# Performance work log

Hardware: AMD Instinct MI355X
Metric: run time of the kernel (lower is better)

The kernel has to match this reference:

```python
import jax, jax.numpy as jnp
import numpy as np

N = 16384      # nodes
E = 524288     # edges (avg degree 32)
F_IN, H1, H2 = 256, 64, 32


def _spmm(edge_src, edge_dst, edge_weight, h):
    """Sparse A @ h with A given as COO edge list: out[i] = sum_{e: src==i} w_e * h[dst_e]."""
    msg = h[edge_dst] * edge_weight[:, None]          # [E, d] gather + scale
    return jax.ops.segment_sum(msg, edge_src, num_segments=N)


def setup_inputs() -> dict:
    key = jax.random.key(0)
    ks = jax.random.split(key, 9)
    x = jax.random.normal(ks[0], (N, F_IN), dtype=jnp.float32)
    edge_src = jax.random.randint(ks[1], (E,), 0, N, dtype=jnp.int32)
    edge_dst = jax.random.randint(ks[2], (E,), 0, N, dtype=jnp.int32)
    edge_weight = jax.random.uniform(ks[3], (E,), dtype=jnp.float32)
    # Xavier-uniform GCN weights
    def xavier(k, shape):
        lim = np.sqrt(6.0 / (shape[0] + shape[1])).astype(np.float32)
        return jax.random.uniform(k, shape, jnp.float32, -lim, lim)
    W1 = xavier(ks[4], (F_IN, H1))
    W2 = xavier(ks[5], (H1, H2))
    W3 = xavier(ks[6], (H1, H2))
    R = jax.random.normal(ks[7], (H2,), dtype=jnp.float32)           # DEDICOM diagonal
    M = jnp.diag(jax.random.normal(ks[8], (H2,), dtype=jnp.float32))  # initialized as diag(randn)
    return dict(x=x, edge_weight=edge_weight, W1=W1, W2=W2, W3=W3, R=R, M=M,
                edge_src=edge_src, edge_dst=edge_dst)


def reference(x, edge_weight, W1, W2, W3, R, M, edge_src, edge_dst):
    # GCN propagation A @ (X @ W); stored activations are never applied in the
    # original ConvGraph.forward, so none are applied here. Eval mode: no
    # dropout, reparameterize returns z_mean.
    h = _spmm(edge_src, edge_dst, edge_weight, x @ W1)        # [N, H1]
    z_mean = _spmm(edge_src, edge_dst, edge_weight, h @ W2)   # [N, H2]
    z_log_std = _spmm(edge_src, edge_dst, edge_weight, h @ W3)
    z = z_mean
    # DEDICOM decoder (act = identity): zt = z @ diag(R) @ M @ diag(R); out = zt @ zt.T
    zt = ((z * R[None, :]) @ M) * R[None, :]                  # diag matmuls -> elementwise scales
    adj_pred = zt @ zt.T                                      # [N, N]
    return adj_pred, z_mean, z_log_std
```

## Files before the change

kernel.cpp:

```cpp
#include <hip/hip_runtime.h>
#include <hip/hip_bf16.h>

#define NN 16384
#define NE 524288
#define FIN 256
#define HH1 64
#define HH2 32

typedef __attribute__((ext_vector_type(8))) short bf16x8;
typedef __attribute__((ext_vector_type(4))) float f32x4;

__global__ __launch_bounds__(256) void zero_ints(int* __restrict__ p, int n) {
  int i = blockIdx.x * 256 + threadIdx.x;
  if (i < n) p[i] = 0;
}

__global__ __launch_bounds__(256) void gemm_xw1(const float* __restrict__ x,
                                                const float* __restrict__ W1,
                                                float* __restrict__ H0) {
  __shared__ float xs[64][65];
  __shared__ float ws[64][65];
  const int t = threadIdx.x;
  const int row0 = blockIdx.x * 64;
  const int tr = t >> 4, tc = t & 15;
  float acc[4][4] = {};
  for (int kc = 0; kc < FIN; kc += 64) {
#pragma unroll
    for (int i = 0; i < 4; ++i) {
      int slot = t + i * 256;
      int r = slot >> 4, c4 = (slot & 15) * 4;
      float4 v = *reinterpret_cast<const float4*>(&x[(size_t)(row0 + r) * FIN + kc + c4]);
      xs[r][c4 + 0] = v.x; xs[r][c4 + 1] = v.y; xs[r][c4 + 2] = v.z; xs[r][c4 + 3] = v.w;
      float4 wv = *reinterpret_cast<const float4*>(&W1[(size_t)(kc + r) * HH1 + c4]);
      ws[r][c4 + 0] = wv.x; ws[r][c4 + 1] = wv.y; ws[r][c4 + 2] = wv.z; ws[r][c4 + 3] = wv.w;
    }
    __syncthreads();
#pragma unroll
    for (int k = 0; k < 64; ++k) {
      float a[4], b[4];
#pragma unroll
      for (int i = 0; i < 4; ++i) a[i] = xs[tr * 4 + i][k];
#pragma unroll
      for (int j = 0; j < 4; ++j) b[j] = ws[k][tc * 4 + j];
#pragma unroll
      for (int i = 0; i < 4; ++i)
#pragma unroll
        for (int j = 0; j < 4; ++j) acc[i][j] += a[i] * b[j];
    }
    __syncthreads();
  }
#pragma unroll
  for (int i = 0; i < 4; ++i) {
    float4 o; o.x = acc[i][0]; o.y = acc[i][1]; o.z = acc[i][2]; o.w = acc[i][3];
    *reinterpret_cast<float4*>(&H0[(size_t)(row0 + tr * 4 + i) * HH1 + tc * 4]) = o;
  }
}

__global__ __launch_bounds__(256) void hist_src(const int* __restrict__ src,
                                                int* __restrict__ cnt) {
  int e = blockIdx.x * 256 + threadIdx.x;
  if (e < NE) atomicAdd(&cnt[src[e]], 1);
}

__global__ __launch_bounds__(256) void scan_offsets(const int* __restrict__ cnt,
                                                    int* __restrict__ off,
                                                    int* __restrict__ cur) {
  __shared__ int sums[256];
  const int t = threadIdx.x;
  const int base = t * 64;
  int s = 0;
  for (int i = 0; i < 64; ++i) s += cnt[base + i];
  sums[t] = s;
  __syncthreads();
  if (t == 0) {
    int run = 0;
    for (int i = 0; i < 256; ++i) { int v = sums[i]; sums[i] = run; run += v; }
  }
  __syncthreads();
  int run = sums[t];
  for (int i = 0; i < 64; ++i) {
    off[base + i] = run;
    cur[base + i] = run;
    run += cnt[base + i];
  }
  if (t == 255) off[NN] = run;
}

__global__ __launch_bounds__(256) void scatter_edges(const int* __restrict__ src,
                                                     const int* __restrict__ dst,
                                                     const float* __restrict__ w,
                                                     int* __restrict__ cur,
                                                     int* __restrict__ sdst,
                                                     float* __restrict__ sw) {
  int e = blockIdx.x * 256 + threadIdx.x;
  if (e < NE) {
    int s = src[e];
    int p = atomicAdd(&cur[s], 1);
    sdst[p] = dst[e];
    sw[p] = w[e];
  }
}

__global__ __launch_bounds__(256) void spmm64(const int* __restrict__ off,
                                              const int* __restrict__ sdst,
                                              const float* __restrict__ sw,
                                              const float* __restrict__ Hin,
                                              float* __restrict__ Hout) {
  const int node = blockIdx.x * 4 + (threadIdx.x >> 6);
  const int lane = threadIdx.x & 63;
  const int beg = off[node], end = off[node + 1];
  float acc = 0.f;
  int e = beg;
  for (; e + 1 < end; e += 2) {
    int d0 = sdst[e], d1 = sdst[e + 1];
    float w0 = sw[e], w1 = sw[e + 1];
    acc += w0 * Hin[(size_t)d0 * 64 + lane];
    acc += w1 * Hin[(size_t)d1 * 64 + lane];
  }
  if (e < end) acc += sw[e] * Hin[(size_t)sdst[e] * 64 + lane];
  Hout[(size_t)node * 64 + lane] = acc;
}

__global__ __launch_bounds__(256) void spmm_out(const int* __restrict__ off,
                                                const int* __restrict__ sdst,
                                                const float* __restrict__ sw,
                                                const float* __restrict__ G,
                                                float* __restrict__ zmean,
                                                float* __restrict__ zlog) {
  const int node = blockIdx.x * 4 + (threadIdx.x >> 6);
  const int lane = threadIdx.x & 63;
  const int beg = off[node], end = off[node + 1];
  float acc = 0.f;
  int e = beg;
  for (; e + 1 < end; e += 2) {
    int d0 = sdst[e], d1 = sdst[e + 1];
    float w0 = sw[e], w1 = sw[e + 1];
    acc += w0 * G[(size_t)d0 * 64 + lane];
    acc += w1 * G[(size_t)d1 * 64 + lane];
  }
  if (e < end) acc += sw[e] * G[(size_t)sdst[e] * 64 + lane];
  if (lane < 32) zmean[(size_t)node * 32 + lane] = acc;
  else           zlog[(size_t)node * 32 + (lane - 32)] = acc;
}

__global__ __launch_bounds__(256) void gemm_h_w23(const float* __restrict__ h1,
                                                  const float* __restrict__ W2,
                                                  const float* __restrict__ W3,
                                                  float* __restrict__ G) {
  __shared__ float wsh[64][64];
  __shared__ float hrow[4][64];
  const int t = threadIdx.x;
  for (int i = t; i < 64 * 32; i += 256) {
    int k = i >> 5, c = i & 31;
    wsh[k][c]      = W2[i];
    wsh[k][c + 32] = W3[i];
  }
  const int node0 = blockIdx.x * 4;
  const int wv = t >> 6, lane = t & 63;
  for (int i = t; i < 4 * 64; i += 256)
    hrow[i >> 6][i & 63] = h1[(size_t)(node0 + (i >> 6)) * 64 + (i & 63)];
  __syncthreads();
  float acc = 0.f;
#pragma unroll
  for (int k = 0; k < 64; ++k) acc += hrow[wv][k] * wsh[k][lane];
  G[(size_t)(node0 + wv) * 64 + lane] = acc;
}

__global__ __launch_bounds__(256) void zt_kernel(const float* __restrict__ zmean,
                                                 const float* __restrict__ R,
                                                 const float* __restrict__ M,
                                                 __hip_bfloat16* __restrict__ ztb) {
  __shared__ float Ms[32][33];
  __shared__ float zr[8][32];
  const int t = threadIdx.x;
  for (int i = t; i < 1024; i += 256) Ms[i >> 5][i & 31] = M[i];
  const int node0 = blockIdx.x * 8;
  const int sub = t >> 5, lane = t & 31;
  zr[sub][lane] = zmean[(size_t)(node0 + sub) * 32 + lane] * R[lane];
  __syncthreads();
  float acc = 0.f;
#pragma unroll
  for (int k = 0; k < 32; ++k) acc += zr[sub][k] * Ms[k][lane];
  ztb[(size_t)(node0 + sub) * 32 + lane] = __float2bfloat16(acc * R[lane]);
}

__global__ __launch_bounds__(256) void adj_mfma(const __hip_bfloat16* __restrict__ ztb,
                                                float* __restrict__ adj) {
  const int wave = threadIdx.x >> 6;
  const int lane = threadIdx.x & 63;
  const int rbase = blockIdx.y * 64 + wave * 16;
  const int cbase = blockIdx.x * 64;
  const int l15 = lane & 15;
  const int kblk = lane >> 4;
  const short* zs = reinterpret_cast<const short*>(ztb);

  bf16x8 a = *reinterpret_cast<const bf16x8*>(&zs[(size_t)(rbase + l15) * 32 + kblk * 8]);

  f32x4 d[4];
#pragma unroll
  for (int tcol = 0; tcol < 4; ++tcol) {
    bf16x8 b = *reinterpret_cast<const bf16x8*>(
        &zs[(size_t)(cbase + tcol * 16 + l15) * 32 + kblk * 8]);
    f32x4 c = {0.f, 0.f, 0.f, 0.f};
    d[tcol] = __builtin_amdgcn_mfma_f32_16x16x32_bf16(a, b, c, 0, 0, 0);
  }

  const int row0 = rbase + kblk * 4;
#pragma unroll
  for (int tcol = 0; tcol < 4; ++tcol) {
    const size_t col = (size_t)(cbase + tcol * 16 + l15);
#pragma unroll
    for (int r = 0; r < 4; ++r) {
      adj[(size_t)(row0 + r) * NN + col] = d[tcol][r];
    }
  }
}

extern "C" void kernel_launch(void* const* d_in, const int* in_sizes, int n_in,
                              void* d_out, int out_size, void* d_ws, size_t ws_size,
                              hipStream_t stream) {
  (void)in_sizes; (void)n_in; (void)out_size; (void)ws_size;

  const float* x   = (const float*)d_in[0];
  const float* ew  = (const float*)d_in[1];
  const float* W1  = (const float*)d_in[2];
  const float* W2  = (const float*)d_in[3];
  const float* W3  = (const float*)d_in[4];
  const float* R   = (const float*)d_in[5];
  const float* M   = (const float*)d_in[6];
  const int* esrc  = (const int*)d_in[7];
  const int* edst  = (const int*)d_in[8];

  float* adj_out   = (float*)d_out;
  float* zmean_out = adj_out + (size_t)NN * NN;
  float* zlog_out  = zmean_out + (size_t)NN * HH2;

  char* p = (char*)d_ws;
  float* H0 = (float*)p;                 p += (size_t)NN * HH1 * 4;
  float* h1 = (float*)p;                 p += (size_t)NN * HH1 * 4;
  float* G  = (float*)p;                 p += (size_t)NN * HH1 * 4;
  __hip_bfloat16* ztb = (__hip_bfloat16*)p; p += (size_t)NN * HH2 * 2;
  int* cnt  = (int*)p;                   p += (size_t)NN * 4;
  int* off  = (int*)p;                   p += (size_t)(NN + 4) * 4;
  int* cur  = (int*)p;                   p += (size_t)NN * 4;
  int* sdst = (int*)p;                   p += (size_t)NE * 4;
  float* sw = (float*)p;                 p += (size_t)NE * 4;

  zero_ints<<<NN / 256, 256, 0, stream>>>(cnt, NN);
  gemm_xw1<<<NN / 64, 256, 0, stream>>>(x, W1, H0);
  hist_src<<<NE / 256, 256, 0, stream>>>(esrc, cnt);
  scan_offsets<<<1, 256, 0, stream>>>(cnt, off, cur);
  scatter_edges<<<NE / 256, 256, 0, stream>>>(esrc, edst, ew, cur, sdst, sw);
  spmm64<<<NN / 4, 256, 0, stream>>>(off, sdst, sw, H0, h1);
  gemm_h_w23<<<NN / 4, 256, 0, stream>>>(h1, W2, W3, G);
  spmm_out<<<NN / 4, 256, 0, stream>>>(off, sdst, sw, G, zmean_out, zlog_out);
  zt_kernel<<<NN / 8, 256, 0, stream>>>(zmean_out, R, M, ztb);

  dim3 g(NN / 64, NN / 64, 1);
  adj_mfma<<<g, 256, 0, stream>>>(ztb, adj_out);
}
```

Measured before the change: 353.9 us.

## Fuse SpMM with dense projections, parallelize scan, retile adjacency MFMA kernel

Fuses the first SpMM with the h@[W2|W3] projection and the second SpMM with the DEDICOM zt transform, removing two launches and the h1 intermediate round trip. The offset scan now uses vectorized loads and wave shuffles instead of a serial loop. The adjacency kernel computes transposed 16x16 tiles so each lane writes contiguous float4 results with nontemporal stores, with each block covering a 128x1024 region. This targets the dominant 1 GiB output write, at the cost of more work per block and fewer blocks.

```diff
diff --git a/kernel.cpp b/kernel.cpp
--- a/kernel.cpp
+++ b/kernel.cpp
@@ -65,23 +65,42 @@
 __global__ __launch_bounds__(256) void scan_offsets(const int* __restrict__ cnt,
                                                     int* __restrict__ off,
                                                     int* __restrict__ cur) {
-  __shared__ int sums[256];
-  const int t = threadIdx.x;
-  const int base = t * 64;
+  __shared__ int wsum[4];
+  __shared__ int wpre[4];
+  const int t = threadIdx.x;
+  const int lane = t & 63, w = t >> 6;
+  int v[64];
+#pragma unroll
+  for (int i = 0; i < 16; ++i) {
+    int4 q = reinterpret_cast<const int4*>(cnt)[t * 16 + i];
+    v[i * 4 + 0] = q.x; v[i * 4 + 1] = q.y; v[i * 4 + 2] = q.z; v[i * 4 + 3] = q.w;
+  }
   int s = 0;
-  for (int i = 0; i < 64; ++i) s += cnt[base + i];
-  sums[t] = s;
+#pragma unroll
+  for (int i = 0; i < 64; ++i) s += v[i];
+  int incl = s;
+#pragma unroll
+  for (int d = 1; d < 64; d <<= 1) {
+    int n = __shfl_up(incl, d, 64);
+    if (lane >= d) incl += n;
+  }
+  if (lane == 63) wsum[w] = incl;
   __syncthreads();
   if (t == 0) {
     int run = 0;
-    for (int i = 0; i < 256; ++i) { int v = sums[i]; sums[i] = run; run += v; }
-  }
-  __syncthreads();
-  int run = sums[t];
-  for (int i = 0; i < 64; ++i) {
-    off[base + i] = run;
-    cur[base + i] = run;
-    run += cnt[base + i];
+    for (int i = 0; i < 4; ++i) { int x = wsum[i]; wpre[i] = run; run += x; }
+  }
+  __syncthreads();
+  int run = incl - s + wpre[w];
+#pragma unroll
+  for (int i = 0; i < 16; ++i) {
+    int4 o;
+    o.x = run; run += v[i * 4 + 0];
+    o.y = run; run += v[i * 4 + 1];
+    o.z = run; run += v[i * 4 + 2];
+    o.w = run; run += v[i * 4 + 3];
+    reinterpret_cast<int4*>(off)[t * 16 + i] = o;
+    reinterpret_cast<int4*>(cur)[t * 16 + i] = o;
   }
   if (t == 255) off[NN] = run;
 }
@@ -101,118 +120,110 @@
   }
 }
 
-__global__ __launch_bounds__(256) void spmm64(const int* __restrict__ off,
+__global__ __launch_bounds__(256) void spmm_g(const int* __restrict__ off,
                                               const int* __restrict__ sdst,
                                               const float* __restrict__ sw,
                                               const float* __restrict__ Hin,
-                                              float* __restrict__ Hout) {
-  const int node = blockIdx.x * 4 + (threadIdx.x >> 6);
-  const int lane = threadIdx.x & 63;
-  const int beg = off[node], end = off[node + 1];
-  float acc = 0.f;
-  int e = beg;
-  for (; e + 1 < end; e += 2) {
-    int d0 = sdst[e], d1 = sdst[e + 1];
-    float w0 = sw[e], w1 = sw[e + 1];
-    acc += w0 * Hin[(size_t)d0 * 64 + lane];
-    acc += w1 * Hin[(size_t)d1 * 64 + lane];
-  }
-  if (e < end) acc += sw[e] * Hin[(size_t)sdst[e] * 64 + lane];
-  Hout[(size_t)node * 64 + lane] = acc;
-}
-
-__global__ __launch_bounds__(256) void spmm_out(const int* __restrict__ off,
-                                                const int* __restrict__ sdst,
-                                                const float* __restrict__ sw,
-                                                const float* __restrict__ G,
-                                                float* __restrict__ zmean,
-                                                float* __restrict__ zlog) {
-  const int node = blockIdx.x * 4 + (threadIdx.x >> 6);
-  const int lane = threadIdx.x & 63;
-  const int beg = off[node], end = off[node + 1];
-  float acc = 0.f;
-  int e = beg;
-  for (; e + 1 < end; e += 2) {
-    int d0 = sdst[e], d1 = sdst[e + 1];
-    float w0 = sw[e], w1 = sw[e + 1];
-    acc += w0 * G[(size_t)d0 * 64 + lane];
-    acc += w1 * G[(size_t)d1 * 64 + lane];
-  }
-  if (e < end) acc += sw[e] * G[(size_t)sdst[e] * 64 + lane];
-  if (lane < 32) zmean[(size_t)node * 32 + lane] = acc;
-  else           zlog[(size_t)node * 32 + (lane - 32)] = acc;
-}
-
-__global__ __launch_bounds__(256) void gemm_h_w23(const float* __restrict__ h1,
-                                                  const float* __restrict__ W2,
-                                                  const float* __restrict__ W3,
-                                                  float* __restrict__ G) {
+                                              const float* __restrict__ W2,
+                                              const float* __restrict__ W3,
+                                              float* __restrict__ G) {
   __shared__ float wsh[64][64];
-  __shared__ float hrow[4][64];
+  __shared__ float hsh[4][64];
   const int t = threadIdx.x;
   for (int i = t; i < 64 * 32; i += 256) {
     int k = i >> 5, c = i & 31;
     wsh[k][c]      = W2[i];
     wsh[k][c + 32] = W3[i];
   }
-  const int node0 = blockIdx.x * 4;
+  const int node = blockIdx.x * 4 + (t >> 6);
+  const int lane = t & 63;
+  const int beg = off[node], end = off[node + 1];
+  float acc = 0.f;
+  int e = beg;
+  for (; e + 4 <= end; e += 4) {
+    int d0 = sdst[e], d1 = sdst[e + 1], d2 = sdst[e + 2], d3 = sdst[e + 3];
+    float w0 = sw[e], w1 = sw[e + 1], w2 = sw[e + 2], w3 = sw[e + 3];
+    acc += w0 * Hin[(size_t)d0 * 64 + lane];
+    acc += w1 * Hin[(size_t)d1 * 64 + lane];
+    acc += w2 * Hin[(size_t)d2 * 64 + lane];
+    acc += w3 * Hin[(size_t)d3 * 64 + lane];
+  }
+  for (; e < end; ++e) acc += sw[e] * Hin[(size_t)sdst[e] * 64 + lane];
+  hsh[t >> 6][lane] = acc;
+  __syncthreads();
+  float g = 0.f;
+#pragma unroll
+  for (int k = 0; k < 64; ++k) g += hsh[t >> 6][k] * wsh[k][lane];
+  G[(size_t)node * 64 + lane] = g;
+}
+
+__global__ __launch_bounds__(256) void spmm_zt(const int* __restrict__ off,
+                                               const int* __restrict__ sdst,
+                                               const float* __restrict__ sw,
+                                               const float* __restrict__ G,
+                                               const float* __restrict__ R,
+                                               const float* __restrict__ M,
+                                               float* __restrict__ zmean,
+                                               float* __restrict__ zlog,
+                                               __hip_bfloat16* __restrict__ ztb) {
+  __shared__ float Ms[32][33];
+  __shared__ float zr[4][32];
+  const int t = threadIdx.x;
+  for (int i = t; i < 1024; i += 256) Ms[i >> 5][i & 31] = M[i];
   const int wv = t >> 6, lane = t & 63;
-  for (int i = t; i < 4 * 64; i += 256)
-    hrow[i >> 6][i & 63] = h1[(size_t)(node0 + (i >> 6)) * 64 + (i & 63)];
-  __syncthreads();
+  const int node = blockIdx.x * 4 + wv;
+  const int beg = off[node], end = off[node + 1];
   float acc = 0.f;
-#pragma unroll
-  for (int k = 0; k < 64; ++k) acc += hrow[wv][k] * wsh[k][lane];
-  G[(size_t)(node0 + wv) * 64 + lane] = acc;
-}
-
-__global__ __launch_bounds__(256) void zt_kernel(const float* __restrict__ zmean,
-                                                 const float* __restrict__ R,
-                                                 const float* __restrict__ M,
-                                                 __hip_bfloat16* __restrict__ ztb) {
-  __shared__ float Ms[32][33];
-  __shared__ float zr[8][32];
-  const int t = threadIdx.x;
-  for (int i = t; i < 1024; i += 256) Ms[i >> 5][i & 31] = M[i];
-  const int node0 = blockIdx.x * 8;
-  const int sub = t >> 5, lane = t & 31;
-  zr[sub][lane] = zmean[(size_t)(node0 + sub) * 32 + lane] * R[lane];
-  __syncthreads();
-  float acc = 0.f;
-#pragma unroll
-  for (int k = 0; k < 32; ++k) acc += zr[sub][k] * Ms[k][lane];
-  ztb[(size_t)(node0 + sub) * 32 + lane] = __float2bfloat16(acc * R[lane]);
+  int e = beg;
+  for (; e + 4 <= end; e += 4) {
+    int d0 = sdst[e], d1 = sdst[e + 1], d2 = sdst[e + 2], d3 = sdst[e + 3];
+    float w0 = sw[e], w1 = sw[e + 1], w2 = sw[e + 2], w3 = sw[e + 3];
+    acc += w0 * G[(size_t)d0 * 64 + lane];
+    acc += w1 * G[(size_t)d1 * 64 + lane];
+    acc += w2 * G[(size_t)d2 * 64 + lane];
+    acc += w3 * G[(size_t)d3 * 64 + lane];
+  }
+  for (; e < end; ++e) acc += sw[e] * G[(size_t)sdst[e] * 64 + lane];
+  if (lane < 32) {
+    zmean[(size_t)node * 32 + lane] = acc;
+    zr[wv][lane] = acc * R[lane];
+  } else {
+    zlog[(size_t)node * 32 + (lane - 32)] = acc;
+  }
+  __syncthreads();
+  if (lane < 32) {
+    float zt = 0.f;
+#pragma unroll
+    for (int k = 0; k < 32; ++k) zt += zr[wv][k] * Ms[k][lane];
+    ztb[(size_t)node * 32 + lane] = __float2bfloat16(zt * R[lane]);
+  }
 }
 
 __global__ __launch_bounds__(256) void adj_mfma(const __hip_bfloat16* __restrict__ ztb,
                                                 float* __restrict__ adj) {
   const int wave = threadIdx.x >> 6;
   const int lane = threadIdx.x & 63;
-  const int rbase = blockIdx.y * 64 + wave * 16;
-  const int cbase = blockIdx.x * 64;
   const int l15 = lane & 15;
   const int kblk = lane >> 4;
+  const int rbase = blockIdx.y * 128 + wave * 32;
+  const int cbase = blockIdx.x * 1024;
   const short* zs = reinterpret_cast<const short*>(ztb);
 
-  bf16x8 a = *reinterpret_cast<const bf16x8*>(&zs[(size_t)(rbase + l15) * 32 + kblk * 8]);
-
-  f32x4 d[4];
-#pragma unroll
-  for (int tcol = 0; tcol < 4; ++tcol) {
-    bf16x8 b = *reinterpret_cast<const bf16x8*>(
-        &zs[(size_t)(cbase + tcol * 16 + l15) * 32 + kblk * 8]);
-    f32x4 c = {0.f, 0.f, 0.f, 0.f};
-    d[tcol] = __builtin_amdgcn_mfma_f32_16x16x32_bf16(a, b, c, 0, 0, 0);
-  }
-
-  const int row0 = rbase + kblk * 4;
-#pragma unroll
-  for (int tcol = 0; tcol < 4; ++tcol) {
-    const size_t col = (size_t)(cbase + tcol * 16 + l15);
-#pragma unroll
-    for (int r = 0; r < 4; ++r) {
-      adj[(size_t)(row0 + r) * NN + col] = d[tcol][r];
-    }
+  bf16x8 b0 = *reinterpret_cast<const bf16x8*>(&zs[(size_t)(rbase + l15) * 32 + kblk * 8]);
+  bf16x8 b1 = *reinterpret_cast<const bf16x8*>(&zs[(size_t)(rbase + 16 + l15) * 32 + kblk * 8]);
+
+  float* p0 = &adj[(size_t)(rbase + l15) * NN + cbase + kblk * 4];
+  float* p1 = &adj[(size_t)(rbase + 16 + l15) * NN + cbase + kblk * 4];
+
+#pragma unroll 4
+  for (int tc = 0; tc < 64; ++tc) {
+    bf16x8 a = *reinterpret_cast<const bf16x8*>(
+        &zs[(size_t)(cbase + tc * 16 + l15) * 32 + kblk * 8]);
+    f32x4 z4 = {0.f, 0.f, 0.f, 0.f};
+    f32x4 d0 = __builtin_amdgcn_mfma_f32_16x16x32_bf16(a, b0, z4, 0, 0, 0);
+    f32x4 d1 = __builtin_amdgcn_mfma_f32_16x16x32_bf16(a, b1, z4, 0, 0, 0);
+    __builtin_nontemporal_store(d0, reinterpret_cast<f32x4*>(p0 + tc * 16));
+    __builtin_nontemporal_store(d1, reinterpret_cast<f32x4*>(p1 + tc * 16));
   }
 }
 
@@ -237,7 +248,6 @@
 
   char* p = (char*)d_ws;
   float* H0 = (float*)p;                 p += (size_t)NN * HH1 * 4;
-  float* h1 = (float*)p;                 p += (size_t)NN * HH1 * 4;
   float* G  = (float*)p;                 p += (size_t)NN * HH1 * 4;
   __hip_bfloat16* ztb = (__hip_bfloat16*)p; p += (size_t)NN * HH2 * 2;
   int* cnt  = (int*)p;                   p += (size_t)NN * 4;
@@ -251,11 +261,10 @@
   hist_src<<<NE / 256, 256, 0, stream>>>(esrc, cnt);
   scan_offsets<<<1, 256, 0, stream>>>(cnt, off, cur);
   scatter_edges<<<NE / 256, 256, 0, stream>>>(esrc, edst, ew, cur, sdst, sw);
-  spmm64<<<NN / 4, 256, 0, stream>>>(off, sdst, sw, H0, h1);
-  gemm_h_w23<<<NN / 4, 256, 0, stream>>>(h1, W2, W3, G);
-  spmm_out<<<NN / 4, 256, 0, stream>>>(off, sdst, sw, G, zmean_out, zlog_out);
-  zt_kernel<<<NN / 8, 256, 0, stream>>>(zmean_out, R, M, ztb);
-
-  dim3 g(NN / 64, NN / 64, 1);
+  spmm_g<<<NN / 4, 256, 0, stream>>>(off, sdst, sw, H0, W2, W3, G);
+  spmm_zt<<<NN / 4, 256, 0, stream>>>(off, sdst, sw, G, R, M,
+                                      zmean_out, zlog_out, ztb);
+
+  dim3 g(NN / 1024, NN / 128, 1);
   adj_mfma<<<g, 256, 0, stream>>>(ztb, adj_out);
 }
```

Result: slower. 549.5 us (+55.3%).
